# Optimization experiments

Measured on AMD Instinct MI355X. Metric: run time of the kernel, lower is better.

Reference implementation:

```python
import jax, jax.numpy as jnp
import numpy as np

N_CTX = 10  # conv_concat is 10*idf -> idf, so the module expects exactly 10 contexts


def setup_inputs() -> dict:
    key = jax.random.key(0)
    ks = jax.random.split(key, 7)
    B, idf, ih, iw = 32, 256, 32, 32
    cdf, L = 512, 128
    inp = {
        "input": jax.random.normal(ks[0], (B, idf, ih, iw), jnp.float32),
        "contexts": jax.random.normal(ks[1], (N_CTX, B, cdf, L), jnp.float32),
        "Wc": jax.random.normal(ks[2], (idf, cdf), jnp.float32) * 0.02,      # conv_context 1x1, no bias
        "Wcat": jax.random.normal(ks[3], (idf, N_CTX * idf), jnp.float32) * 0.02,  # conv_concat 1x1, no bias
        "Wb": jax.random.normal(ks[4], (idf,), jnp.float32) * 0.02,          # conv_b weight applied to ones -> bias
        "gamma": jnp.ones((idf,), jnp.float32),
        "beta": jnp.zeros((idf,), jnp.float32),
    }
    return inp


def reference(input, contexts, Wc, Wcat, Wb, gamma, beta):
    B, idf, ih, iw = input.shape
    Q = ih * iw
    # target: [B, Q, idf]
    targetT = jnp.transpose(input.reshape(B, idf, Q), (0, 2, 1))
    # project all 10 contexts at once: conv1x1(cdf->idf) == matmul over channel dim
    sourceT = jnp.einsum('dc,nbcl->nbdl', Wc, contexts)          # [N, B, idf, L]
    # attention weights: bmm(targetT, sourceT) then softmax over source dim
    w = jax.nn.softmax(jnp.einsum('bqd,nbdl->nbql', targetT, sourceT), axis=-1)  # [N,B,Q,L]
    attn = jnp.einsum('nbql,nbdl->nbqd', w, sourceT)             # [N, B, Q, idf]
    # torch.cat over last dim in loop order i=0..9 -> interleave as [B,Q,N*idf]
    cat = jnp.transpose(attn, (1, 2, 0, 3)).reshape(B, Q, N_CTX * idf)
    # conv_concat (1x1) over channels + conv_b(ones) bias
    x = jnp.einsum('ef,bqf->bqe', Wcat, cat) + Wb                # [B, Q, idf]
    x = jax.nn.relu(x) + targetT
    # LayerNorm over idf, eps=0, affine
    mu = jnp.mean(x, axis=-1, keepdims=True)
    var = jnp.mean(jnp.square(x - mu), axis=-1, keepdims=True)
    return (x - mu) / jnp.sqrt(var) * gamma + beta
```

## Files before the change

kernel.cpp:

```cpp
#include <hip/hip_runtime.h>
#include <cstdint>

typedef unsigned short u16;
typedef unsigned int   u32;
typedef __bf16 bf16x8 __attribute__((ext_vector_type(8)));
typedef float  f32x4  __attribute__((ext_vector_type(4)));

#define NCTX 10
#define BSZ  32
#define IDF  256
#define QSZ  1024
#define CDF  512
#define LSZ  128

__device__ __forceinline__ u16 f2bf(float f) {
    u32 u = __float_as_uint(f);
    u += 0x7FFFu + ((u >> 16) & 1u);
    return (u16)(u >> 16);
}
__device__ __forceinline__ float bf2f(u16 h) {
    return __uint_as_float(((u32)h) << 16);
}

union U4V { uint4 u; bf16x8 v; };

__device__ __forceinline__ bf16x8 ldg16(const u16* p) {
    U4V t; t.u = *(const uint4*)p; return t.v;
}
__device__ __forceinline__ bf16x8 lds16(const u16* p) {
    U4V t; t.u = *(const uint4*)p; return t.v;
}
__device__ __forceinline__ bf16x8 pack8(const float* f) {
    U4V t;
    t.u.x = (u32)f2bf(f[0]) | ((u32)f2bf(f[1]) << 16);
    t.u.y = (u32)f2bf(f[2]) | ((u32)f2bf(f[3]) << 16);
    t.u.z = (u32)f2bf(f[4]) | ((u32)f2bf(f[5]) << 16);
    t.u.w = (u32)f2bf(f[6]) | ((u32)f2bf(f[7]) << 16);
    return t.v;
}
__device__ __forceinline__ f32x4 mfma16(bf16x8 a, bf16x8 b, f32x4 c) {
    return __builtin_amdgcn_mfma_f32_16x16x32_bf16(a, b, c, 0, 0, 0);
}

__device__ __forceinline__ void gl_lds16(const u16* g, u16* l) {
    __builtin_amdgcn_global_load_lds(
        (__attribute__((address_space(1))) void*)(g),
        (__attribute__((address_space(3))) void*)(l), 16, 0, 0);
}

__device__ __forceinline__ void vm_wait4() {
    asm volatile("s_waitcnt vmcnt(4)" ::: "memory");
    __builtin_amdgcn_sched_barrier(0);
}
__device__ __forceinline__ void vm_wait0() {
    asm volatile("s_waitcnt vmcnt(0)" ::: "memory");
    __builtin_amdgcn_sched_barrier(0);
}
__device__ __forceinline__ void mid_bar()  {
    __builtin_amdgcn_s_barrier();
    asm volatile("" ::: "memory");
}
__device__ __forceinline__ void end_bar()  {
    asm volatile("" ::: "memory");
    __builtin_amdgcn_s_barrier();
    asm volatile("" ::: "memory");
}
__device__ __forceinline__ void lg_bar()   {
    asm volatile("s_waitcnt lgkmcnt(0)" ::: "memory");
    __builtin_amdgcn_sched_barrier(0);
    __builtin_amdgcn_s_barrier();
    asm volatile("" ::: "memory");
}

__device__ __forceinline__ int swz_cg(int L) {
    return (((L & 3) + ((L >> 3) & 3)) & 3) * 8;
}
__device__ __forceinline__ int swz_off(int row, int quad) {
    return row * 32 + ((quad - (row >> 1)) & 3) * 8;
}

__device__ __forceinline__ void stage_ph1(u16* buf, const u16* sttH, const u16* sttL,
                                          int c0, int w, int L) {
    const int rr = L >> 2, cg = swz_cg(L);
#pragma unroll
    for (int j = 0; j < 4; ++j) {
        const int c = 4 * w + j;
        const int hi = (c < 8);
        const int ch = hi ? c : c - 8;
        const u16* src = (hi ? sttH : sttL) + (long)(ch * 16 + rr) * IDF + c0 + cg;
        gl_lds16(src, buf + (hi ? 0 : 4096) + ch * 512);
    }
}

__device__ __forceinline__ void stage_256(u16* buf, const u16* gbase, int stride,
                                          int c0, int w, int L) {
    const int rr = L >> 2, cg = swz_cg(L);
#pragma unroll
    for (int j = 0; j < 4; ++j) {
        const int c = 4 * w + j;
        const u16* src = gbase + (long)(c * 16 + rr) * stride + c0 + cg;
        gl_lds16(src, buf + c * 512);
    }
}

__global__ __launch_bounds__(256) void k1a_conv(const float* __restrict__ Wc,
                                                const float* __restrict__ Wcat,
                                                u16* __restrict__ Wc_hi,
                                                u16* __restrict__ Wc_lo,
                                                u16* __restrict__ Wcat_bf) {
    int i = blockIdx.x * 256 + threadIdx.x;
    if (i < IDF * CDF) {
        float f = Wc[i];
        u16 h = f2bf(f);
        Wc_hi[i] = h;
        Wc_lo[i] = f2bf(f - bf2f(h));
    } else {
        int j = i - IDF * CDF;
        Wcat_bf[j] = f2bf(Wcat[j]);
    }
}

__global__ __launch_bounds__(256) void k1b_tgt(const float* __restrict__ input,
                                               u16* __restrict__ T_hi,
                                               u16* __restrict__ T_lo) {
    __shared__ float t[32][33];
    const int tx = threadIdx.x, ty = threadIdx.y;
    const int qt = blockIdx.x, dt = blockIdx.y, b = blockIdx.z;
#pragma unroll
    for (int k = 0; k < 4; ++k)
        t[ty + 8 * k][tx] = input[((long)b * IDF + dt * 32 + ty + 8 * k) * QSZ + qt * 32 + tx];
    __syncthreads();
#pragma unroll
    for (int k = 0; k < 4; ++k) {
        int q = qt * 32 + ty + 8 * k;
        float f = t[tx][ty + 8 * k];
        u16 h = f2bf(f);
        long o = ((long)b * QSZ + q) * IDF + dt * 32 + tx;
        T_hi[o] = h;
        T_lo[o] = f2bf(f - bf2f(h));
    }
}

__global__ __launch_bounds__(256) void k1c_ctx(const float* __restrict__ ctx,
                                               u16* __restrict__ ctxT) {
    __shared__ float t[32][33];
    const int tx = threadIdx.x, ty = threadIdx.y;
    const int lt = blockIdx.x, ct = blockIdx.y, nb = blockIdx.z;
    const long ib = (long)nb * CDF * LSZ;
#pragma unroll
    for (int k = 0; k < 4; ++k)
        t[ty + 8 * k][tx] = ctx[ib + (long)(ct * 32 + ty + 8 * k) * LSZ + lt * 32 + tx];
    __syncthreads();
    const long ob = (long)nb * LSZ * CDF;
#pragma unroll
    for (int k = 0; k < 4; ++k)
        ctxT[ob + (long)(lt * 32 + ty + 8 * k) * CDF + ct * 32 + tx] = f2bf(t[tx][ty + 8 * k]);
}

__global__ __launch_bounds__(256, 2) void k2_src(const u16* __restrict__ Wc_hi,
                                                 const u16* __restrict__ Wc_lo,
                                                 const u16* __restrict__ ctxT,
                                                 u16* __restrict__ sTT_hi,
                                                 u16* __restrict__ sTT_lo,
                                                 u16* __restrict__ s_dl) {
    __shared__ u16 bounce[128 * 136];
    const int tid = threadIdx.x;
    const int L = tid & 63, w = tid >> 6;
    const int wd = w >> 1, wl = w & 1, lr = L & 15, quad = L >> 4;
    const int dbase = blockIdx.x * 128;
    const int nb = blockIdx.y;
    const u16* ctxb = ctxT + (long)nb * LSZ * CDF;

    const f32x4 vz = {0.f, 0.f, 0.f, 0.f};
    f32x4 acc[4][4];
#pragma unroll
    for (int m = 0; m < 4; ++m)
#pragma unroll
        for (int nn = 0; nn < 4; ++nn) acc[m][nn] = vz;

    for (int kc = 0; kc < 16; ++kc) {
        const int c0 = kc * 32 + quad * 8;
        bf16x8 aH[4], aL[4], bb[4];
#pragma unroll
        for (int m = 0; m < 4; ++m) {
            const int d = dbase + 64 * wd + 16 * m + lr;
            aH[m] = ldg16(Wc_hi + d * CDF + c0);
            aL[m] = ldg16(Wc_lo + d * CDF + c0);
        }
#pragma unroll
        for (int nn = 0; nn < 4; ++nn) {
            const int l = 64 * wl + 16 * nn + lr;
            bb[nn] = ldg16(ctxb + l * CDF + c0);
        }
#pragma unroll
        for (int m = 0; m < 4; ++m)
#pragma unroll
            for (int nn = 0; nn < 4; ++nn) {
                acc[m][nn] = mfma16(aH[m], bb[nn], acc[m][nn]);
                acc[m][nn] = mfma16(aL[m], bb[nn], acc[m][nn]);
            }
    }

#pragma unroll
    for (int m = 0; m < 4; ++m)
#pragma unroll
        for (int nn = 0; nn < 4; ++nn)
#pragma unroll
            for (int r = 0; r < 4; ++r) {
                const int d = 64 * wd + 16 * m + 4 * quad + r;
                const int l = 64 * wl + 16 * nn + lr;
                bounce[l * 136 + d] = f2bf(acc[m][nn][r]);
            }
    __syncthreads();
    for (int i = tid; i < 2048; i += 256) {
        const int l = i >> 4, g = (i & 15) * 8;
        *(uint4*)(sTT_hi + ((long)nb * LSZ + l) * IDF + dbase + g) =
            *(const uint4*)(bounce + l * 136 + g);
    }
    __syncthreads();
#pragma unroll
    for (int m = 0; m < 4; ++m)
#pragma unroll
        for (int nn = 0; nn < 4; ++nn)
#pragma unroll
            for (int r = 0; r < 4; ++r) {
                const int d = 64 * wd + 16 * m + 4 * quad + r;
                const int l = 64 * wl + 16 * nn + lr;
                float c = acc[m][nn][r];
                u16 h = f2bf(c);
                bounce[l * 136 + d] = f2bf(c - bf2f(h));
            }
    __syncthreads();
    for (int i = tid; i < 2048; i += 256) {
        const int l = i >> 4, g = (i & 15) * 8;
        *(uint4*)(sTT_lo + ((long)nb * LSZ + l) * IDF + dbase + g) =
            *(const uint4*)(bounce + l * 136 + g);
    }
    __syncthreads();
#pragma unroll
    for (int m = 0; m < 4; ++m)
#pragma unroll
        for (int nn = 0; nn < 4; ++nn)
#pragma unroll
            for (int r = 0; r < 4; ++r) {
                const int d = 64 * wd + 16 * m + 4 * quad + r;
                const int l = 64 * wl + 16 * nn + lr;
                bounce[d * 136 + l] = f2bf(acc[m][nn][r]);
            }
    __syncthreads();
    for (int i = tid; i < 2048; i += 256) {
        const int d = i >> 4, g = (i & 15) * 8;
        *(uint4*)(s_dl + ((long)nb * IDF + dbase + d) * LSZ + g) =
            *(const uint4*)(bounce + d * 136 + g);
    }
}

__global__ __launch_bounds__(256, 2) void k3_attn(
    const u16* __restrict__ T_hi, const u16* __restrict__ T_lo,
    const u16* __restrict__ sTT_hi, const u16* __restrict__ sTT_lo,
    const u16* __restrict__ s_dl, const u16* __restrict__ Wcat_bf,
    const float* __restrict__ Wb, const float* __restrict__ gam_p,
    const float* __restrict__ bet_p, float* __restrict__ out)
{
    __shared__ __align__(16) u16 ST[2][8192];
    __shared__ float S[64 * 132];
    __shared__ float redA[256];
    __shared__ float redB[256];
    u16* attnL = (u16*)S;

    const int tid = threadIdx.x;
    const int L = tid & 63, w = tid >> 6;
    const int wq = w >> 1, wh = w & 1, lr = L & 15, quad = L >> 4;
    const int b = blockIdx.y;
    const int bq = b * QSZ + blockIdx.x * 64;

    const f32x4 vz = {0.f, 0.f, 0.f, 0.f};
    f32x4 x_acc[2][8];
#pragma unroll
    for (int m = 0; m < 2; ++m)
#pragma unroll
        for (int nn = 0; nn < 8; ++nn) x_acc[m][nn] = vz;

    stage_ph1(ST[0], sTT_hi + (long)b * (LSZ * IDF), sTT_lo + (long)b * (LSZ * IDF),
              0, w, L);

    for (int n = 0; n < NCTX; ++n) {
        const int nb = n * BSZ + b;
        const u16* sttH = sTT_hi + (long)nb * (LSZ * IDF);
        const u16* sttL = sTT_lo + (long)nb * (LSZ * IDF);
        const u16* sdl  = s_dl  + (long)nb * (IDF * LSZ);
        const u16* wcat = Wcat_bf + n * IDF;

        f32x4 s_acc[2][4];
#pragma unroll
        for (int m = 0; m < 2; ++m)
#pragma unroll
            for (int nn = 0; nn < 4; ++nn) s_acc[m][nn] = vz;

        for (int kc = 0; kc < 8; ++kc) {
            const int cur = kc & 1;
            const int c0 = kc * 32 + quad * 8;
            bf16x8 aH[2], aL[2];
#pragma unroll
            for (int m = 0; m < 2; ++m) {
                const int ro = (bq + 32 * wq + 16 * m + lr) * IDF + c0;
                aH[m] = ldg16(T_hi + ro);
                aL[m] = ldg16(T_lo + ro);
            }
            asm volatile("" ::: "memory");
            if (kc < 7) stage_ph1(ST[cur ^ 1], sttH, sttL, (kc + 1) * 32, w, L);
            else        stage_256(ST[cur ^ 1], sdl, LSZ, 0, w, L);
            vm_wait4();
            mid_bar();

            const u16* Bh = ST[cur];
            const u16* Bl = ST[cur] + 4096;
            bf16x8 bH[4], bL[4];
#pragma unroll
            for (int nn = 0; nn < 4; ++nn) {
                const int off = swz_off(64 * wh + 16 * nn + lr, quad);
                bH[nn] = lds16(Bh + off);
                bL[nn] = lds16(Bl + off);
            }
#pragma unroll
            for (int m = 0; m < 2; ++m)
#pragma unroll
                for (int nn = 0; nn < 4; ++nn) {
                    s_acc[m][nn] = mfma16(aH[m], bH[nn], s_acc[m][nn]);
                    s_acc[m][nn] = mfma16(aH[m], bL[nn], s_acc[m][nn]);
                    s_acc[m][nn] = mfma16(aL[m], bH[nn], s_acc[m][nn]);
                }
            end_bar();
        }

#pragma unroll
        for (int m = 0; m < 2; ++m)
#pragma unroll
            for (int nn = 0; nn < 4; ++nn)
#pragma unroll
                for (int r = 0; r < 4; ++r)
                    S[(32 * wq + 16 * m + 4 * quad + r) * 132 + 64 * wh + 16 * nn + lr] =
                        s_acc[m][nn][r];
        lg_bar();

        {
            const int row = tid >> 2, sg = (tid & 3) * 32;
            float* sp = S + row * 132 + sg;
            float mx = sp[0];
#pragma unroll
            for (int i = 1; i < 32; ++i) mx = fmaxf(mx, sp[i]);
            redA[row * 4 + (tid & 3)] = mx;
            lg_bar();
            const float rm = fmaxf(fmaxf(redA[row * 4], redA[row * 4 + 1]),
                                   fmaxf(redA[row * 4 + 2], redA[row * 4 + 3]));
            float sm = 0.f;
#pragma unroll
            for (int i = 0; i < 32; ++i) {
                float e = __expf(sp[i] - rm);
                sp[i] = e;
                sm += e;
            }
            redB[row * 4 + (tid & 3)] = sm;
            lg_bar();
        }

        f32x4 a_acc[2][8];
#pragma unroll
        for (int m = 0; m < 2; ++m)
#pragma unroll
            for (int nn = 0; nn < 8; ++nn) a_acc[m][nn] = vz;

        for (int kc = 0; kc < 4; ++kc) {
            const int cur = kc & 1;
            if (kc < 3) stage_256(ST[cur ^ 1], sdl, LSZ, (kc + 1) * 32, w, L);
            else        stage_256(ST[cur ^ 1], wcat, NCTX * IDF, 0, w, L);
            vm_wait4();
            mid_bar();

            const int l0 = kc * 32 + quad * 8;
            bf16x8 af[2];
#pragma unroll
            for (int m = 0; m < 2; ++m)
                af[m] = pack8(S + (32 * wq + 16 * m + lr) * 132 + l0);
            const u16* Bd = ST[cur];
#pragma unroll
            for (int nn = 0; nn < 8; ++nn) {
                const int off = swz_off(128 * wh + 16 * nn + lr, quad);
                bf16x8 bf = lds16(Bd + off);
#pragma unroll
                for (int m = 0; m < 2; ++m)
                    a_acc[m][nn] = mfma16(af[m], bf, a_acc[m][nn]);
            }
            end_bar();
        }

        float invr[2][4];
#pragma unroll
        for (int m = 0; m < 2; ++m)
#pragma unroll
            for (int r = 0; r < 4; ++r) {
                const int row = 32 * wq + 16 * m + 4 * quad + r;
                invr[m][r] = 1.0f / (redB[row * 4] + redB[row * 4 + 1] +
                                     redB[row * 4 + 2] + redB[row * 4 + 3]);
            }
#pragma unroll
        for (int m = 0; m < 2; ++m)
#pragma unroll
            for (int nn = 0; nn < 8; ++nn)
#pragma unroll
                for (int r = 0; r < 4; ++r) {
                    const int row = 32 * wq + 16 * m + 4 * quad + r;
                    const int col = 128 * wh + 16 * nn + lr;
                    attnL[row * 264 + col] = f2bf(a_acc[m][nn][r] * invr[m][r]);
                }
        lg_bar();

        for (int kc = 0; kc < 8; ++kc) {
            const int cur = kc & 1;
            if (kc < 7) stage_256(ST[cur ^ 1], wcat, NCTX * IDF, (kc + 1) * 32, w, L);
            else if (n < NCTX - 1) {
                const u16* nH = sTT_hi + (long)((n + 1) * BSZ + b) * (LSZ * IDF);
                const u16* nL = sTT_lo + (long)((n + 1) * BSZ + b) * (LSZ * IDF);
                stage_ph1(ST[cur ^ 1], nH, nL, 0, w, L);
            }
            vm_wait4();
            mid_bar();

            const int d0 = kc * 32 + quad * 8;
            bf16x8 af[2];
#pragma unroll
            for (int m = 0; m < 2; ++m) {
                U4V t;
                t.u = *(const uint4*)(attnL + (32 * wq + 16 * m + lr) * 264 + d0);
                af[m] = t.v;
            }
            const u16* Wt = ST[cur];
#pragma unroll
            for (int nn = 0; nn < 8; ++nn) {
                const int off = swz_off(128 * wh + 16 * nn + lr, quad);
                bf16x8 bf = lds16(Wt + off);
#pragma unroll
                for (int m = 0; m < 2; ++m)
                    x_acc[m][nn] = mfma16(af[m], bf, x_acc[m][nn]);
            }
            end_bar();
        }
    }
    vm_wait0();

    float gv[8], bv[8], wv[8];
    int ec[8];
#pragma unroll
    for (int nn = 0; nn < 8; ++nn) {
        ec[nn] = 128 * wh + 16 * nn + lr;
        wv[nn] = Wb[ec[nn]];
        gv[nn] = gam_p[ec[nn]];
        bv[nn] = bet_p[ec[nn]];
    }
#pragma unroll
    for (int m = 0; m < 2; ++m)
#pragma unroll
        for (int r = 0; r < 4; ++r) {
            const int row = 32 * wq + 16 * m + 4 * quad + r;
            const u16* th = T_hi + (long)(bq + row) * IDF;
            const u16* tl = T_lo + (long)(bq + row) * IDF;
#pragma unroll
            for (int nn = 0; nn < 8; ++nn) {
                float resid = bf2f(th[ec[nn]]) + bf2f(tl[ec[nn]]);
                x_acc[m][nn][r] = fmaxf(x_acc[m][nn][r] + wv[nn], 0.f) + resid;
            }
        }
    float s1[2][4], s2[2][4];
#pragma unroll
    for (int m = 0; m < 2; ++m)
#pragma unroll
        for (int r = 0; r < 4; ++r) {
            float a = 0.f, q2 = 0.f;
#pragma unroll
            for (int nn = 0; nn < 8; ++nn) {
                float v = x_acc[m][nn][r];
                a += v;
                q2 += v * v;
            }
            s1[m][r] = a;
            s2[m][r] = q2;
        }
#pragma unroll
    for (int off = 1; off <= 8; off <<= 1)
#pragma unroll
        for (int m = 0; m < 2; ++m)
#pragma unroll
            for (int r = 0; r < 4; ++r) {
                s1[m][r] += __shfl_xor(s1[m][r], off);
                s2[m][r] += __shfl_xor(s2[m][r], off);
            }
    if (lr == 0) {
#pragma unroll
        for (int m = 0; m < 2; ++m)
#pragma unroll
            for (int r = 0; r < 4; ++r) {
                const int row = 32 * wq + 16 * m + 4 * quad + r;
                redA[row * 4 + wh * 2]     = s1[m][r];
                redA[row * 4 + wh * 2 + 1] = s2[m][r];
            }
    }
    __syncthreads();
#pragma unroll
    for (int m = 0; m < 2; ++m)
#pragma unroll
        for (int r = 0; r < 4; ++r) {
            const int row = 32 * wq + 16 * m + 4 * quad + r;
            const float S1 = redA[row * 4] + redA[row * 4 + 2];
            const float S2 = redA[row * 4 + 1] + redA[row * 4 + 3];
            const float mu = S1 * (1.f / 256.f);
            const float rs = rsqrtf(S2 * (1.f / 256.f) - mu * mu);
            float* op = out + (long)(bq + row) * IDF;
#pragma unroll
            for (int nn = 0; nn < 8; ++nn)
                op[ec[nn]] = (x_acc[m][nn][r] - mu) * rs * gv[nn] + bv[nn];
        }
}

extern "C" void kernel_launch(void* const* d_in, const int* in_sizes, int n_in,
                              void* d_out, int out_size, void* d_ws, size_t ws_size,
                              hipStream_t stream) {
    const float* input    = (const float*)d_in[0];
    const float* contexts = (const float*)d_in[1];
    const float* Wc       = (const float*)d_in[2];
    const float* Wcat     = (const float*)d_in[3];
    const float* Wb       = (const float*)d_in[4];
    const float* gamma    = (const float*)d_in[5];
    const float* beta     = (const float*)d_in[6];
    float* out = (float*)d_out;

    char* ws = (char*)d_ws;
    size_t off = 0;
    u16* Wc_hi   = (u16*)(ws + off); off += (size_t)IDF * CDF * 2;
    u16* Wc_lo   = (u16*)(ws + off); off += (size_t)IDF * CDF * 2;
    u16* Wcat_bf = (u16*)(ws + off); off += (size_t)IDF * NCTX * IDF * 2;
    u16* T_hi    = (u16*)(ws + off); off += (size_t)BSZ * QSZ * IDF * 2;
    u16* T_lo    = (u16*)(ws + off); off += (size_t)BSZ * QSZ * IDF * 2;
    u16* ctxT    = (u16*)(ws + off); off += (size_t)NCTX * BSZ * LSZ * CDF * 2;
    u16* sTT_hi  = (u16*)(ws + off); off += (size_t)NCTX * BSZ * LSZ * IDF * 2;
    u16* sTT_lo  = (u16*)(ws + off); off += (size_t)NCTX * BSZ * LSZ * IDF * 2;
    u16* s_dl    = (u16*)(ws + off); off += (size_t)NCTX * BSZ * IDF * LSZ * 2;
    (void)in_sizes; (void)n_in; (void)out_size; (void)ws_size;

    k1a_conv<<<3072, 256, 0, stream>>>(Wc, Wcat, Wc_hi, Wc_lo, Wcat_bf);
    k1b_tgt<<<dim3(QSZ / 32, IDF / 32, BSZ), dim3(32, 8), 0, stream>>>(input, T_hi, T_lo);
    k1c_ctx<<<dim3(LSZ / 32, CDF / 32, NCTX * BSZ), dim3(32, 8), 0, stream>>>(contexts, ctxT);
    k2_src<<<dim3(2, NCTX * BSZ), 256, 0, stream>>>(Wc_hi, Wc_lo, ctxT, sTT_hi, sTT_lo, s_dl);
    k3_attn<<<dim3(QSZ / 64, BSZ), 256, 0, stream>>>(T_hi, T_lo, sTT_hi, sTT_lo, s_dl,
                                                     Wcat_bf, Wb, gamma, beta, out);
}
```

Measured before the change: 528.1 us.

## Vectorize transpose kernels, LDS-stage context tiles in k2, swap k3 grid order

The fp32 transpose/convert kernels now use 64-row tiles with float4 loads and 16-byte packed bf16 stores instead of scalar accesses. The source-projection kernel stages the context operand through double-buffered LDS with async global-to-LDS loads, replacing direct global reads. The attention kernel's grid is reordered so consecutive blocks cover different batches rather than consecutive query tiles of one batch, which changes L2 locality for per-batch source data. The LDS pipeline adds barriers per k-step and more shared memory in k2, which may lower occupancy.

```diff
diff --git a/kernel.cpp b/kernel.cpp
--- a/kernel.cpp
+++ b/kernel.cpp
@@ -52,6 +52,10 @@
     asm volatile("s_waitcnt vmcnt(4)" ::: "memory");
     __builtin_amdgcn_sched_barrier(0);
 }
+__device__ __forceinline__ void vm_wait2() {
+    asm volatile("s_waitcnt vmcnt(2)" ::: "memory");
+    __builtin_amdgcn_sched_barrier(0);
+}
 __device__ __forceinline__ void vm_wait0() {
     asm volatile("s_waitcnt vmcnt(0)" ::: "memory");
     __builtin_amdgcn_sched_barrier(0);
@@ -98,6 +102,17 @@
 #pragma unroll
     for (int j = 0; j < 4; ++j) {
         const int c = 4 * w + j;
+        const u16* src = gbase + (long)(c * 16 + rr) * stride + c0 + cg;
+        gl_lds16(src, buf + c * 512);
+    }
+}
+
+__device__ __forceinline__ void stage_128(u16* buf, const u16* gbase, int stride,
+                                          int c0, int w, int L) {
+    const int rr = L >> 2, cg = swz_cg(L);
+#pragma unroll
+    for (int j = 0; j < 2; ++j) {
+        const int c = 2 * w + j;
         const u16* src = gbase + (long)(c * 16 + rr) * stride + c0 + cg;
         gl_lds16(src, buf + c * 512);
     }
@@ -123,38 +138,61 @@
 __global__ __launch_bounds__(256) void k1b_tgt(const float* __restrict__ input,
                                                u16* __restrict__ T_hi,
                                                u16* __restrict__ T_lo) {
-    __shared__ float t[32][33];
-    const int tx = threadIdx.x, ty = threadIdx.y;
+    __shared__ float ts[64][33];
+    const int tid = threadIdx.x;
     const int qt = blockIdx.x, dt = blockIdx.y, b = blockIdx.z;
-#pragma unroll
-    for (int k = 0; k < 4; ++k)
-        t[ty + 8 * k][tx] = input[((long)b * IDF + dt * 32 + ty + 8 * k) * QSZ + qt * 32 + tx];
-    __syncthreads();
-#pragma unroll
-    for (int k = 0; k < 4; ++k) {
-        int q = qt * 32 + ty + 8 * k;
-        float f = t[tx][ty + 8 * k];
-        u16 h = f2bf(f);
-        long o = ((long)b * QSZ + q) * IDF + dt * 32 + tx;
-        T_hi[o] = h;
-        T_lo[o] = f2bf(f - bf2f(h));
+    {
+        const int dl = tid >> 2, q0 = (tid & 3) * 8;
+        const float* src = input + ((long)(b * IDF + dt * 64 + dl)) * QSZ + qt * 32 + q0;
+        float4 v0 = *(const float4*)src;
+        float4 v1 = *(const float4*)(src + 4);
+        ts[dl][q0 + 0] = v0.x; ts[dl][q0 + 1] = v0.y;
+        ts[dl][q0 + 2] = v0.z; ts[dl][q0 + 3] = v0.w;
+        ts[dl][q0 + 4] = v1.x; ts[dl][q0 + 5] = v1.y;
+        ts[dl][q0 + 6] = v1.z; ts[dl][q0 + 7] = v1.w;
+    }
+    __syncthreads();
+    {
+        const int ql = tid >> 3, d8 = (tid & 7) * 8;
+        u16 hi[8], lo[8];
+#pragma unroll
+        for (int i = 0; i < 8; ++i) {
+            float f = ts[d8 + i][ql];
+            hi[i] = f2bf(f);
+            lo[i] = f2bf(f - bf2f(hi[i]));
+        }
+        const long o = ((long)(b * QSZ + qt * 32 + ql)) * IDF + dt * 64 + d8;
+        *(uint4*)(T_hi + o) = *(const uint4*)hi;
+        *(uint4*)(T_lo + o) = *(const uint4*)lo;
     }
 }
 
 __global__ __launch_bounds__(256) void k1c_ctx(const float* __restrict__ ctx,
                                                u16* __restrict__ ctxT) {
-    __shared__ float t[32][33];
-    const int tx = threadIdx.x, ty = threadIdx.y;
+    __shared__ float ts[64][33];
+    const int tid = threadIdx.x;
     const int lt = blockIdx.x, ct = blockIdx.y, nb = blockIdx.z;
     const long ib = (long)nb * CDF * LSZ;
-#pragma unroll
-    for (int k = 0; k < 4; ++k)
-        t[ty + 8 * k][tx] = ctx[ib + (long)(ct * 32 + ty + 8 * k) * LSZ + lt * 32 + tx];
-    __syncthreads();
-    const long ob = (long)nb * LSZ * CDF;
-#pragma unroll
-    for (int k = 0; k < 4; ++k)
-        ctxT[ob + (long)(lt * 32 + ty + 8 * k) * CDF + ct * 32 + tx] = f2bf(t[tx][ty + 8 * k]);
+    {
+        const int cl = tid >> 2, l0 = (tid & 3) * 8;
+        const float* src = ctx + ib + (long)(ct * 64 + cl) * LSZ + lt * 32 + l0;
+        float4 v0 = *(const float4*)src;
+        float4 v1 = *(const float4*)(src + 4);
+        ts[cl][l0 + 0] = v0.x; ts[cl][l0 + 1] = v0.y;
+        ts[cl][l0 + 2] = v0.z; ts[cl][l0 + 3] = v0.w;
+        ts[cl][l0 + 4] = v1.x; ts[cl][l0 + 5] = v1.y;
+        ts[cl][l0 + 6] = v1.z; ts[cl][l0 + 7] = v1.w;
+    }
+    __syncthreads();
+    {
+        const int ll = tid >> 3, c8 = (tid & 7) * 8;
+        u16 o8[8];
+#pragma unroll
+        for (int i = 0; i < 8; ++i) o8[i] = f2bf(ts[c8 + i][ll]);
+        const long ob = (long)nb * LSZ * CDF;
+        *(uint4*)(ctxT + ob + (long)(lt * 32 + ll) * CDF + ct * 64 + c8) =
+            *(const uint4*)o8;
+    }
 }
 
 __global__ __launch_bounds__(256, 2) void k2_src(const u16* __restrict__ Wc_hi,
@@ -164,6 +202,7 @@
                                                  u16* __restrict__ sTT_lo,
                                                  u16* __restrict__ s_dl) {
     __shared__ u16 bounce[128 * 136];
+    __shared__ __align__(16) u16 BST[2][4096];
     const int tid = threadIdx.x;
     const int L = tid & 63, w = tid >> 6;
     const int wd = w >> 1, wl = w & 1, lr = L & 15, quad = L >> 4;
@@ -178,20 +217,31 @@
 #pragma unroll
         for (int nn = 0; nn < 4; ++nn) acc[m][nn] = vz;
 
+    stage_128(BST[0], ctxb, CDF, 0, w, L);
+
     for (int kc = 0; kc < 16; ++kc) {
+        const int cur = kc & 1;
         const int c0 = kc * 32 + quad * 8;
-        bf16x8 aH[4], aL[4], bb[4];
+        bf16x8 aH[4], aL[4];
 #pragma unroll
         for (int m = 0; m < 4; ++m) {
             const int d = dbase + 64 * wd + 16 * m + lr;
             aH[m] = ldg16(Wc_hi + d * CDF + c0);
             aL[m] = ldg16(Wc_lo + d * CDF + c0);
         }
-#pragma unroll
-        for (int nn = 0; nn < 4; ++nn) {
-            const int l = 64 * wl + 16 * nn + lr;
-            bb[nn] = ldg16(ctxb + l * CDF + c0);
-        }
+        asm volatile("" ::: "memory");
+        if (kc < 15) {
+            stage_128(BST[cur ^ 1], ctxb, CDF, (kc + 1) * 32, w, L);
+            vm_wait2();
+        } else {
+            vm_wait0();
+        }
+        mid_bar();
+
+        bf16x8 bb[4];
+#pragma unroll
+        for (int nn = 0; nn < 4; ++nn)
+            bb[nn] = lds16(BST[cur] + swz_off(64 * wl + 16 * nn + lr, quad));
 #pragma unroll
         for (int m = 0; m < 4; ++m)
 #pragma unroll
@@ -199,6 +249,7 @@
                 acc[m][nn] = mfma16(aH[m], bb[nn], acc[m][nn]);
                 acc[m][nn] = mfma16(aL[m], bb[nn], acc[m][nn]);
             }
+        end_bar();
     }
 
 #pragma unroll
@@ -271,8 +322,8 @@
     const int tid = threadIdx.x;
     const int L = tid & 63, w = tid >> 6;
     const int wq = w >> 1, wh = w & 1, lr = L & 15, quad = L >> 4;
-    const int b = blockIdx.y;
-    const int bq = b * QSZ + blockIdx.x * 64;
+    const int b = blockIdx.x;
+    const int bq = b * QSZ + blockIdx.y * 64;
 
     const f32x4 vz = {0.f, 0.f, 0.f, 0.f};
     f32x4 x_acc[2][8];
@@ -547,9 +598,9 @@
     (void)in_sizes; (void)n_in; (void)out_size; (void)ws_size;
 
     k1a_conv<<<3072, 256, 0, stream>>>(Wc, Wcat, Wc_hi, Wc_lo, Wcat_bf);
-    k1b_tgt<<<dim3(QSZ / 32, IDF / 32, BSZ), dim3(32, 8), 0, stream>>>(input, T_hi, T_lo);
-    k1c_ctx<<<dim3(LSZ / 32, CDF / 32, NCTX * BSZ), dim3(32, 8), 0, stream>>>(contexts, ctxT);
+    k1b_tgt<<<dim3(QSZ / 32, IDF / 64, BSZ), 256, 0, stream>>>(input, T_hi, T_lo);
+    k1c_ctx<<<dim3(LSZ / 32, CDF / 64, NCTX * BSZ), 256, 0, stream>>>(contexts, ctxT);
     k2_src<<<dim3(2, NCTX * BSZ), 256, 0, stream>>>(Wc_hi, Wc_lo, ctxT, sTT_hi, sTT_lo, s_dl);
-    k3_attn<<<dim3(QSZ / 64, BSZ), 256, 0, stream>>>(T_hi, T_lo, sTT_hi, sTT_lo, s_dl,
+    k3_attn<<<dim3(BSZ, QSZ / 64), 256, 0, stream>>>(T_hi, T_lo, sTT_hi, sTT_lo, s_dl,
                                                      Wcat_bf, Wb, gamma, beta, out);
 }
```

Result: faster. 502.0 us (-4.9%).
